# Performance work log

Measured on AMD Instinct MI355X. Metric: run time of the kernel, lower is better.

## Reference

```python
import jax, jax.numpy as jnp
import numpy as np

N_NODES = 50000


def _degree_norm(src, dst, n):
    # symmetric GCN normalization with self-loops already appended
    deg = jax.ops.segment_sum(jnp.ones(src.shape[0], jnp.float32), dst, num_segments=n)
    dinv = jnp.where(deg > 0, jax.lax.rsqrt(deg), 0.0)
    return dinv[src] * dinv[dst]  # [E_full]


def _gcn_layer(x, W, b, src, dst, norm, n):
    h = x @ W                                  # [N, out]
    msgs = h[src] * norm[:, None]              # gather + scale, [E_full, out]
    out = jax.ops.segment_sum(msgs, dst, num_segments=n)
    return out + b


def setup_inputs() -> dict:
    key = jax.random.key(0)
    k1, k2, k3, k4 = jax.random.split(key, 4)
    n, e, d_in, d_out = N_NODES, 800000, 256, 128
    x = jax.random.normal(k1, (n, d_in), jnp.float32)
    edge_index = jax.random.randint(k2, (2, e), 0, n, dtype=jnp.int64)
    W1 = jax.random.normal(k3, (d_in, 2 * d_out), jnp.float32) / np.sqrt(d_in)
    b1 = jnp.zeros((2 * d_out,), jnp.float32)
    W2 = jax.random.normal(k4, (2 * d_out, d_out), jnp.float32) / np.sqrt(2 * d_out)
    b2 = jnp.zeros((d_out,), jnp.float32)
    return {"x": x, "edge_index": edge_index, "W1": W1, "b1": b1, "W2": W2, "b2": b2}


def reference(x, edge_index, W1, b1, W2, b2):
    n = x.shape[0]
    loops = jnp.arange(n, dtype=edge_index.dtype)
    src = jnp.concatenate([edge_index[0], loops])
    dst = jnp.concatenate([edge_index[1], loops])
    norm = _degree_norm(src, dst, n)
    h = jax.nn.relu(_gcn_layer(x, W1, b1, src, dst, norm, n))
    h = jax.nn.relu(_gcn_layer(h, W2, b2, src, dst, norm, n))
    return h
```

## Files before the change

### kernel.cpp

```cpp
#include <hip/hip_runtime.h>
#include <hip/hip_bf16.h>


typedef __attribute__((ext_vector_type(8))) short bf16x8;
typedef __attribute__((ext_vector_type(8))) unsigned short u16x8;
typedef __attribute__((ext_vector_type(4))) float f32x4;

__device__ inline float bf2f(unsigned short u) {
    return __uint_as_float(((unsigned)u) << 16);
}
__device__ inline unsigned short f2bf(float f) {
    unsigned x = __float_as_uint(f);
    unsigned r = (x + 0x7fffu + ((x >> 16) & 1u)) >> 16;
    return (unsigned short)r;
}

#define NBIN 512

__global__ void degree_kernel(const int* __restrict__ dst, unsigned* __restrict__ deg, int E) {
    int e = blockIdx.x * blockDim.x + threadIdx.x;
    if (e < E) atomicAdd(&deg[dst[e]], 1u);
}

__global__ __launch_bounds__(256) void dinv_hist_kernel(const unsigned* __restrict__ deg,
                                                        float* __restrict__ dinv,
                                                        int* __restrict__ hist, int N) {
    __shared__ int lh[NBIN];
    const int t = threadIdx.x;
#pragma unroll
    for (int i = 0; i < NBIN / 256; i++) lh[t + i * 256] = 0;
    __syncthreads();
    int idx = blockIdx.x * 256 + t;
    if (idx < N) {
        unsigned d = deg[idx];
        dinv[idx] = rsqrtf((float)(d + 1u));
        int b = (int)d; if (b > NBIN - 1) b = NBIN - 1;
        atomicAdd(&lh[NBIN - 1 - b], 1);
    }
    __syncthreads();
#pragma unroll
    for (int i = 0; i < NBIN / 256; i++) {
        int v = lh[t + i * 256];
        if (v) atomicAdd(&hist[t + i * 256], v);
    }
}

__global__ void scan_bins_kernel(const int* __restrict__ hist,
                                 int* __restrict__ binstart,
                                 int* __restrict__ bincur,
                                 int* __restrict__ edgebase,
                                 int* __restrict__ rowptr, int N) {
    const int t = threadIdx.x;
    int cn = 0, ce = 0;
    for (int b = 0; b < NBIN; b += 64) {
        int i = b + t;
        int cnt = hist[i];
        int d = NBIN - 1 - i;
        int d8 = (d + 7) & ~7;
        int en = cnt * d8;
        int xn = cnt, xe = en;
#pragma unroll
        for (int off = 1; off < 64; off <<= 1) {
            int yn = __shfl_up(xn, off, 64);
            int ye = __shfl_up(xe, off, 64);
            if (t >= off) { xn += yn; xe += ye; }
        }
        binstart[i] = cn + xn - cnt;
        bincur[i]   = cn + xn - cnt;
        edgebase[i] = ce + xe - en;
        cn += __shfl(xn, 63, 64);
        ce += __shfl(xe, 63, 64);
    }
    if (t == 0) rowptr[N] = ce;
}

__global__ __launch_bounds__(256) void place_fused_kernel(
    const unsigned* __restrict__ deg,
    int* __restrict__ bincur,
    const int* __restrict__ binstart,
    const int* __restrict__ edgebase,
    int* __restrict__ perm,
    int* __restrict__ rowptr, int* __restrict__ cursor,
    unsigned short* __restrict__ col, int N) {
    __shared__ int lh[NBIN];
    __shared__ int base[NBIN];
    const int t = threadIdx.x;
#pragma unroll
    for (int i = 0; i < NBIN / 256; i++) lh[t + i * 256] = 0;
    __syncthreads();
    int idx = blockIdx.x * 256 + t;
    int bin = 0, lrank = 0;
    if (idx < N) {
        int b = (int)deg[idx]; if (b > NBIN - 1) b = NBIN - 1;
        bin = NBIN - 1 - b;
        lrank = atomicAdd(&lh[bin], 1);
    }
    __syncthreads();
#pragma unroll
    for (int i = 0; i < NBIN / 256; i++) {
        int v = lh[t + i * 256];
        if (v) base[t + i * 256] = atomicAdd(&bincur[t + i * 256], v);
    }
    __syncthreads();
    if (idx < N) {
        int pos = base[bin] + lrank;
        int d = NBIN - 1 - bin;
        int d8 = (d + 7) & ~7;
        int rp = edgebase[bin] + (pos - binstart[bin]) * d8;
        perm[pos] = idx;
        rowptr[pos] = rp;
        cursor[idx] = rp;
        for (int k = d; k < d8; k++) col[rp + k] = (unsigned short)N;
    }
}

__global__ __launch_bounds__(256) void fill_kernel(const int* __restrict__ src,
                                                   const int* __restrict__ dst,
                                                   int* __restrict__ cursor,
                                                   unsigned short* __restrict__ col, int E) {
    int e = blockIdx.x * blockDim.x + threadIdx.x;
    if (e < E) {
        int d = dst[e];
        int pos = atomicAdd(&cursor[d], 1);
        col[pos] = (unsigned short)src[e];
    }
}

__global__ __launch_bounds__(256) void convwt_pad_kernel(
    const float* __restrict__ W1, const float* __restrict__ W2,
    unsigned short* __restrict__ w1t, unsigned short* __restrict__ w2t,
    unsigned short* __restrict__ h1b, unsigned short* __restrict__ h2b,
    int DIN, int H, int DOUT, int Np1) {
    int id = blockIdx.x * 256 + threadIdx.x;
    int n1 = DIN * H;
    int n2 = H * DOUT;
    if (id < n1) {
        int k = id / H, n = id % H;
        w1t[(long)n * DIN + k] = f2bf(W1[id]);
    } else if (id < n1 + n2) {
        int q = id - n1;
        int k = q / DOUT, n = q % DOUT;
        w2t[(long)n * H + k] = f2bf(W2[q]);
    } else if (id < n1 + n2 + 384) {
        int q = id - n1 - n2;
        if (q < 256) {
            int c = q >> 5, f = q & 31;
            h1b[((size_t)c * Np1 + (Np1 - 1)) * 32 + f] = 0;
        } else {
            int q2 = q - 256;
            int c = q2 >> 5, f = q2 & 31;
            h2b[((size_t)c * Np1 + (Np1 - 1)) * 32 + f] = 0;
        }
    }
}

#define GBM 128
#define GBN 128
#define GBK 64
__global__ __launch_bounds__(256) void gemm_x_bf16(const float* __restrict__ X,
                                                   const float* __restrict__ dinv,
                                                   const unsigned short* __restrict__ BT,
                                                   unsigned short* __restrict__ C,
                                                   int M, int Nc, int K, int ldm) {
    __shared__ __align__(16) unsigned short As[GBM * GBK];
    __shared__ __align__(16) unsigned short Bs[GBN * GBK];
    const int t = threadIdx.x;
    const int lane = t & 63;
    const int w = t >> 6;
    const int row0 = blockIdx.x * GBM;
    const int col0 = blockIdx.y * GBN;
    const int rb = (w >> 1) * 64;
    const int cb = (w & 1) * 64;

    f32x4 acc[4][4] = {};

    for (int kb = 0; kb < K; kb += GBK) {
#pragma unroll
        for (int i = 0; i < 4; i++) {
            int p = i * 256 + t;
            int row = p >> 3;
            int slot = p & 7;
            int chunk = slot ^ (row & 7);
            int grow = row0 + row;
            if (grow >= M) grow = M - 1;
            const float* sp = X + (size_t)grow * K + kb + chunk * 8;
            f32x4 v0 = *(const f32x4*)sp;
            f32x4 v1 = *(const f32x4*)(sp + 4);
            float ds = dinv[grow];
            u16x8 o;
#pragma unroll
            for (int j = 0; j < 4; j++) { o[j] = f2bf(v0[j] * ds); o[j + 4] = f2bf(v1[j] * ds); }
            *(u16x8*)&As[p * 8] = o;
        }
#pragma unroll
        for (int i = 0; i < 4; i++) {
            int p = i * 256 + t;
            int row = p >> 3;
            int slot = p & 7;
            int chunk = slot ^ (row & 7);
            const unsigned short* src = BT + (size_t)(col0 + row) * K + kb + chunk * 8;
            __builtin_amdgcn_global_load_lds(
                (const __attribute__((address_space(1))) void*)src,
                (__attribute__((address_space(3))) void*)&Bs[p * 8], 16, 0, 0);
        }
        asm volatile("s_waitcnt vmcnt(0)" ::: "memory");
        __syncthreads();

#pragma unroll
        for (int ks = 0; ks < 2; ks++) {
            int kq = ks * 4 + (lane >> 4);
            int rsel = lane & 15;
            bf16x8 af[4], bfr[4];
#pragma unroll
            for (int mt = 0; mt < 4; mt++) {
                int m = rb + mt * 16 + rsel;
                int slot = kq ^ (m & 7);
                af[mt] = *(const bf16x8*)&As[m * GBK + slot * 8];
            }
#pragma unroll
            for (int nt = 0; nt < 4; nt++) {
                int n = cb + nt * 16 + rsel;
                int slot = kq ^ (n & 7);
                bfr[nt] = *(const bf16x8*)&Bs[n * GBK + slot * 8];
            }
#pragma unroll
            for (int mt = 0; mt < 4; mt++)
#pragma unroll
                for (int nt = 0; nt < 4; nt++)
                    acc[mt][nt] = __builtin_amdgcn_mfma_f32_16x16x32_bf16(
                        af[mt], bfr[nt], acc[mt][nt], 0, 0, 0);
        }
        __syncthreads();
    }

#pragma unroll
    for (int mt = 0; mt < 4; mt++) {
#pragma unroll
        for (int nt = 0; nt < 4; nt++) {
            int gcol = col0 + cb + nt * 16 + (lane & 15);
            int c = gcol >> 5;
            int fo = gcol & 31;
            int grow0 = row0 + rb + mt * 16 + 4 * (lane >> 4);
#pragma unroll
            for (int r = 0; r < 4; r++) {
                int g = grow0 + r;
                if (g < M)
                    C[((size_t)c * ldm + g) * 32 + fo] = f2bf(acc[mt][nt][r]);
            }
        }
    }
}

template <int CH>
__global__ __launch_bounds__(256) void gemm_bf16(const unsigned short* __restrict__ A,
                                                 const unsigned short* __restrict__ BT,
                                                 unsigned short* __restrict__ C,
                                                 int M, int Nc, int K, int ldm) {
    __shared__ __align__(16) unsigned short As[GBM * GBK];
    __shared__ __align__(16) unsigned short Bs[GBN * GBK];
    const int t = threadIdx.x;
    const int lane = t & 63;
    const int w = t >> 6;
    const int row0 = blockIdx.x * GBM;
    const int col0 = blockIdx.y * GBN;
    const int rb = (w >> 1) * 64;
    const int cb = (w & 1) * 64;

    f32x4 acc[4][4] = {};

    for (int kb = 0; kb < K; kb += GBK) {
#pragma unroll
        for (int i = 0; i < 4; i++) {
            int p = i * 256 + t;
            int row = p >> 3;
            int slot = p & 7;
            int chunk = slot ^ (row & 7);
            int grow = row0 + row;
            if (grow >= M) grow = M - 1;
            const unsigned short* src = A + (size_t)grow * K + kb + chunk * 8;
            __builtin_amdgcn_global_load_lds(
                (const __attribute__((address_space(1))) void*)src,
                (__attribute__((address_space(3))) void*)&As[p * 8], 16, 0, 0);
        }
#pragma unroll
        for (int i = 0; i < 4; i++) {
            int p = i * 256 + t;
            int row = p >> 3;
            int slot = p & 7;
            int chunk = slot ^ (row & 7);
            const unsigned short* src = BT + (size_t)(col0 + row) * K + kb + chunk * 8;
            __builtin_amdgcn_global_load_lds(
                (const __attribute__((address_space(1))) void*)src,
                (__attribute__((address_space(3))) void*)&Bs[p * 8], 16, 0, 0);
        }
        asm volatile("s_waitcnt vmcnt(0)" ::: "memory");
        __syncthreads();

#pragma unroll
        for (int ks = 0; ks < 2; ks++) {
            int kq = ks * 4 + (lane >> 4);
            int rsel = lane & 15;
            bf16x8 af[4], bfr[4];
#pragma unroll
            for (int mt = 0; mt < 4; mt++) {
                int m = rb + mt * 16 + rsel;
                int slot = kq ^ (m & 7);
                af[mt] = *(const bf16x8*)&As[m * GBK + slot * 8];
            }
#pragma unroll
            for (int nt = 0; nt < 4; nt++) {
                int n = cb + nt * 16 + rsel;
                int slot = kq ^ (n & 7);
                bfr[nt] = *(const bf16x8*)&Bs[n * GBK + slot * 8];
            }
#pragma unroll
            for (int mt = 0; mt < 4; mt++)
#pragma unroll
                for (int nt = 0; nt < 4; nt++)
                    acc[mt][nt] = __builtin_amdgcn_mfma_f32_16x16x32_bf16(
                        af[mt], bfr[nt], acc[mt][nt], 0, 0, 0);
        }
        __syncthreads();
    }

#pragma unroll
    for (int mt = 0; mt < 4; mt++) {
#pragma unroll
        for (int nt = 0; nt < 4; nt++) {
            int gcol = col0 + cb + nt * 16 + (lane & 15);
            int c = gcol / CH;
            int fo = gcol % CH;
            int grow0 = row0 + rb + mt * 16 + 4 * (lane >> 4);
#pragma unroll
            for (int r = 0; r < 4; r++) {
                int g = grow0 + r;
                if (g < M)
                    C[((size_t)c * ldm + g) * CH + fo] = f2bf(acc[mt][nt][r]);
            }
        }
    }
}

template <int CH, int NCH, bool OUT_BF16>
__global__ __launch_bounds__(512) void gather_cm_kernel(
    const unsigned short* __restrict__ h_cm,
    const int* __restrict__ rowptr,
    const unsigned short* __restrict__ col,
    const int* __restrict__ perm,
    const float* __restrict__ dinv,
    const float* __restrict__ bias,
    void* __restrict__ out,
    int Nn, int F) {
    constexpr int LF = CH / 8;
    constexpr int NS = 64 / LF;
    constexpr int NPB = NS * 8;
    const int chunk = blockIdx.x % NCH;
    const int g = blockIdx.x / NCH;
    const int w = threadIdx.x >> 6;
    const int lane = threadIdx.x & 63;
    const int fl = lane & (LF - 1);
    const int ns = lane / LF;
    const int idx = g * NPB + w * NS + ns;
    const bool valid = idx < Nn;
    const int cidx = valid ? idx : Nn - 1;
    const int node = perm[cidx];

    const unsigned short* hc = h_cm + (size_t)chunk * (Nn + 1) * CH;
    const int beg = rowptr[cidx];
    const int nit = (rowptr[cidx + 1] - beg) >> 3;
    const float ddst = dinv[node];
    const int fo = fl * 8;

    float a0[8] = {}, a1[8] = {};
    const unsigned short* cp = col + beg;
    u16x8 cv = *(const u16x8*)cp;
    for (int it = 0; it < nit; ++it) {
        int s0 = cv[0], s1 = cv[1], s2 = cv[2], s3 = cv[3];
        int s4 = cv[4], s5 = cv[5], s6 = cv[6], s7 = cv[7];
        u16x8 u0 = *(const u16x8*)(hc + s0 * CH + fo);
        u16x8 u1 = *(const u16x8*)(hc + s1 * CH + fo);
        u16x8 u2 = *(const u16x8*)(hc + s2 * CH + fo);
        u16x8 u3 = *(const u16x8*)(hc + s3 * CH + fo);
        u16x8 u4 = *(const u16x8*)(hc + s4 * CH + fo);
        u16x8 u5 = *(const u16x8*)(hc + s5 * CH + fo);
        u16x8 u6 = *(const u16x8*)(hc + s6 * CH + fo);
        u16x8 u7 = *(const u16x8*)(hc + s7 * CH + fo);
        cp += 8;
        cv = *(const u16x8*)cp;
#pragma unroll
        for (int j = 0; j < 8; j++) {
            a0[j] += (bf2f(u0[j]) + bf2f(u1[j])) + (bf2f(u2[j]) + bf2f(u3[j]));
            a1[j] += (bf2f(u4[j]) + bf2f(u5[j])) + (bf2f(u6[j]) + bf2f(u7[j]));
        }
    }

    if (valid) {
        u16x8 us = *(const u16x8*)(hc + node * CH + fo);
        const int f0g = chunk * CH + fo;
        f32x4 bv0 = *(const f32x4*)(bias + f0g);
        f32x4 bv1 = *(const f32x4*)(bias + f0g + 4);
        float v[8];
#pragma unroll
        for (int j = 0; j < 8; j++) {
            float b = (j < 4) ? bv0[j] : bv1[j - 4];
            float s = (a0[j] + a1[j]) + bf2f(us[j]);
            v[j] = fmaxf(fmaf(s, ddst, b), 0.f);
        }
        if (OUT_BF16) {
            u16x8 o;
#pragma unroll
            for (int j = 0; j < 8; j++) o[j] = f2bf(v[j] * ddst);
            *(u16x8*)((unsigned short*)out + (size_t)node * F + f0g) = o;
        } else {
            f32x4 o0, o1;
#pragma unroll
            for (int j = 0; j < 4; j++) { o0[j] = v[j]; o1[j] = v[j + 4]; }
            float* op = (float*)out + (size_t)node * F + f0g;
            *(f32x4*)op = o0;
            *(f32x4*)(op + 4) = o1;
        }
    }
}

extern "C" void kernel_launch(void* const* d_in, const int* in_sizes, int n_in,
                              void* d_out, int out_size, void* d_ws, size_t ws_size,
                              hipStream_t stream) {
    const float* x  = (const float*)d_in[0];
    const int* ei   = (const int*)d_in[1];
    const float* W1 = (const float*)d_in[2];
    const float* b1 = (const float*)d_in[3];
    const float* W2 = (const float*)d_in[4];
    const float* b2 = (const float*)d_in[5];

    const int DIN = 256;
    const int N = in_sizes[0] / DIN;
    const int E = in_sizes[1] / 2;
    const int H = in_sizes[3];
    const int DOUT = in_sizes[5];

    const int* src = ei;
    const int* dst = ei + E;

    char* ws = (char*)d_ws;
    unsigned* deg = (unsigned*)ws;                   ws += (size_t)N * 4;
    int* hist     = (int*)ws;                        ws += NBIN * 4;
    float* dinv   = (float*)ws;                      ws += (size_t)N * 4;
    int* rowptr   = (int*)ws;                        ws += (size_t)(N + 4) * 4;
    int* binstart = (int*)ws;                        ws += NBIN * 4;
    int* bincur   = (int*)ws;                        ws += NBIN * 4;
    int* edgebase = (int*)ws;                        ws += NBIN * 4;
    int* perm     = (int*)ws;                        ws += (size_t)N * 4;
    int* cursor   = (int*)ws;                        ws += (size_t)N * 4;
    unsigned short* col = (unsigned short*)ws;       ws += (size_t)(E + 8 * N + 64) * 2;
    unsigned short* w1t = (unsigned short*)ws;       ws += (size_t)DIN * H * 2;
    unsigned short* w2t = (unsigned short*)ws;       ws += (size_t)H * DOUT * 2;
    unsigned short* h1b = (unsigned short*)ws;       ws += (size_t)(N + 1) * H * 2 + 1024;
    unsigned short* y1b = (unsigned short*)ws;       ws += (size_t)N * H * 2;
    unsigned short* h2b = (unsigned short*)ws;       ws += (size_t)(N + 1) * DOUT * 2 + 1024;
    float* outp = (float*)d_out;

    hipMemsetAsync(deg, 0, (size_t)N * 4 + NBIN * 4, stream);
    degree_kernel<<<(E + 255) / 256, 256, 0, stream>>>(dst, deg, E);
    dinv_hist_kernel<<<(N + 255) / 256, 256, 0, stream>>>(deg, dinv, hist, N);
    scan_bins_kernel<<<1, 64, 0, stream>>>(hist, binstart, bincur, edgebase, rowptr, N);
    place_fused_kernel<<<(N + 255) / 256, 256, 0, stream>>>(
        deg, bincur, binstart, edgebase, perm, rowptr, cursor, col, N);
    fill_kernel<<<(E + 255) / 256, 256, 0, stream>>>(src, dst, cursor, col, E);

    {
        int tot = DIN * H + H * DOUT + 384;
        convwt_pad_kernel<<<(tot + 255) / 256, 256, 0, stream>>>(
            W1, W2, w1t, w2t, h1b, h2b, DIN, H, DOUT, N + 1);
    }

    {
        dim3 grid((N + GBM - 1) / GBM, H / GBN);
        gemm_x_bf16<<<grid, 256, 0, stream>>>(x, dinv, w1t, h1b, N, H, DIN, N + 1);
    }
    {
        constexpr int NPB1 = (64 / (32 / 8)) * 8;
        gather_cm_kernel<32, 8, true><<<8 * ((N + NPB1 - 1) / NPB1), 512, 0, stream>>>(
            h1b, rowptr, col, perm, dinv, b1, y1b, N, H);
    }

    {
        dim3 grid((N + GBM - 1) / GBM, DOUT / GBN);
        gemm_bf16<32><<<grid, 256, 0, stream>>>(y1b, w2t, h2b, N, DOUT, H, N + 1);
    }
    {
        constexpr int NPB2 = (64 / (32 / 8)) * 8;
        gather_cm_kernel<32, 4, false><<<4 * ((N + NPB2 - 1) / NPB2), 512, 0, stream>>>(
            h2b, rowptr, col, perm, dinv, b2, outp, N, DOUT);
    }
}
```

Measured before the change: 313.5 us.

## Fold bin scan into placement kernel and compute full layer-1 width per GEMM block

The single-wave scan_bins kernel is removed. Each place_fused block now recomputes the prefix scan of the degree histogram into shared memory and reserves slots through a zeroed binres counter, which saves one launch and its serial dependency. The first-layer GEMM now has each block compute both 128-column tiles of the 256-wide output, so the fp32 X tile is loaded and converted to bf16 once instead of twice. The cost is double the accumulator registers and B shared memory, which may lower occupancy, plus a redundant scan in every placement block.

```diff
diff --git a/kernel.cpp b/kernel.cpp
--- a/kernel.cpp
+++ b/kernel.cpp
@@ -45,49 +45,42 @@
     }
 }
 
-__global__ void scan_bins_kernel(const int* __restrict__ hist,
-                                 int* __restrict__ binstart,
-                                 int* __restrict__ bincur,
-                                 int* __restrict__ edgebase,
-                                 int* __restrict__ rowptr, int N) {
-    const int t = threadIdx.x;
-    int cn = 0, ce = 0;
-    for (int b = 0; b < NBIN; b += 64) {
-        int i = b + t;
-        int cnt = hist[i];
-        int d = NBIN - 1 - i;
-        int d8 = (d + 7) & ~7;
-        int en = cnt * d8;
-        int xn = cnt, xe = en;
-#pragma unroll
-        for (int off = 1; off < 64; off <<= 1) {
-            int yn = __shfl_up(xn, off, 64);
-            int ye = __shfl_up(xe, off, 64);
-            if (t >= off) { xn += yn; xe += ye; }
-        }
-        binstart[i] = cn + xn - cnt;
-        bincur[i]   = cn + xn - cnt;
-        edgebase[i] = ce + xe - en;
-        cn += __shfl(xn, 63, 64);
-        ce += __shfl(xe, 63, 64);
-    }
-    if (t == 0) rowptr[N] = ce;
-}
-
 __global__ __launch_bounds__(256) void place_fused_kernel(
     const unsigned* __restrict__ deg,
-    int* __restrict__ bincur,
-    const int* __restrict__ binstart,
-    const int* __restrict__ edgebase,
+    const int* __restrict__ hist,
+    int* __restrict__ binres,
     int* __restrict__ perm,
     int* __restrict__ rowptr, int* __restrict__ cursor,
     unsigned short* __restrict__ col, int N) {
     __shared__ int lh[NBIN];
     __shared__ int base[NBIN];
+    __shared__ int binstartL[NBIN];
+    __shared__ int edgebaseL[NBIN];
     const int t = threadIdx.x;
 #pragma unroll
     for (int i = 0; i < NBIN / 256; i++) lh[t + i * 256] = 0;
     __syncthreads();
+    if (t < 64) {
+        int cn = 0, ce = 0;
+        for (int b = 0; b < NBIN; b += 64) {
+            int i = b + t;
+            int cnt = hist[i];
+            int d = NBIN - 1 - i;
+            int d8 = (d + 7) & ~7;
+            int en = cnt * d8;
+            int xn = cnt, xe = en;
+#pragma unroll
+            for (int off = 1; off < 64; off <<= 1) {
+                int yn = __shfl_up(xn, off, 64);
+                int ye = __shfl_up(xe, off, 64);
+                if (t >= off) { xn += yn; xe += ye; }
+            }
+            binstartL[i] = cn + xn - cnt;
+            edgebaseL[i] = ce + xe - en;
+            cn += __shfl(xn, 63, 64);
+            ce += __shfl(xe, 63, 64);
+        }
+    }
     int idx = blockIdx.x * 256 + t;
     int bin = 0, lrank = 0;
     if (idx < N) {
@@ -96,17 +89,19 @@
         lrank = atomicAdd(&lh[bin], 1);
     }
     __syncthreads();
+    if (blockIdx.x == 0 && t == 0) rowptr[N] = edgebaseL[NBIN - 1];
 #pragma unroll
     for (int i = 0; i < NBIN / 256; i++) {
         int v = lh[t + i * 256];
-        if (v) base[t + i * 256] = atomicAdd(&bincur[t + i * 256], v);
+        if (v) base[t + i * 256] = binstartL[t + i * 256] +
+                                   atomicAdd(&binres[t + i * 256], v);
     }
     __syncthreads();
     if (idx < N) {
         int pos = base[bin] + lrank;
         int d = NBIN - 1 - bin;
         int d8 = (d + 7) & ~7;
-        int rp = edgebase[bin] + (pos - binstart[bin]) * d8;
+        int rp = edgebaseL[bin] + (pos - binstartL[bin]) * d8;
         perm[pos] = idx;
         rowptr[pos] = rp;
         cursor[idx] = rp;
@@ -161,18 +156,17 @@
                                                    const float* __restrict__ dinv,
                                                    const unsigned short* __restrict__ BT,
                                                    unsigned short* __restrict__ C,
-                                                   int M, int Nc, int K, int ldm) {
+                                                   int M, int K, int ldm) {
     __shared__ __align__(16) unsigned short As[GBM * GBK];
-    __shared__ __align__(16) unsigned short Bs[GBN * GBK];
+    __shared__ __align__(16) unsigned short Bs[2][GBN * GBK];
     const int t = threadIdx.x;
     const int lane = t & 63;
     const int w = t >> 6;
     const int row0 = blockIdx.x * GBM;
-    const int col0 = blockIdx.y * GBN;
     const int rb = (w >> 1) * 64;
     const int cb = (w & 1) * 64;
 
-    f32x4 acc[4][4] = {};
+    f32x4 acc[2][4][4] = {};
 
     for (int kb = 0; kb < K; kb += GBK) {
 #pragma unroll
@@ -193,16 +187,18 @@
             *(u16x8*)&As[p * 8] = o;
         }
 #pragma unroll
-        for (int i = 0; i < 4; i++) {
-            int p = i * 256 + t;
-            int row = p >> 3;
-            int slot = p & 7;
-            int chunk = slot ^ (row & 7);
-            const unsigned short* src = BT + (size_t)(col0 + row) * K + kb + chunk * 8;
-            __builtin_amdgcn_global_load_lds(
-                (const __attribute__((address_space(1))) void*)src,
-                (__attribute__((address_space(3))) void*)&Bs[p * 8], 16, 0, 0);
-        }
+        for (int ct = 0; ct < 2; ct++)
+#pragma unroll
+            for (int i = 0; i < 4; i++) {
+                int p = i * 256 + t;
+                int row = p >> 3;
+                int slot = p & 7;
+                int chunk = slot ^ (row & 7);
+                const unsigned short* src = BT + (size_t)(ct * GBN + row) * K + kb + chunk * 8;
+                __builtin_amdgcn_global_load_lds(
+                    (const __attribute__((address_space(1))) void*)src,
+                    (__attribute__((address_space(3))) void*)&Bs[ct][p * 8], 16, 0, 0);
+            }
         asm volatile("s_waitcnt vmcnt(0)" ::: "memory");
         __syncthreads();
 
@@ -210,7 +206,7 @@
         for (int ks = 0; ks < 2; ks++) {
             int kq = ks * 4 + (lane >> 4);
             int rsel = lane & 15;
-            bf16x8 af[4], bfr[4];
+            bf16x8 af[4];
 #pragma unroll
             for (int mt = 0; mt < 4; mt++) {
                 int m = rb + mt * 16 + rsel;
@@ -218,37 +214,42 @@
                 af[mt] = *(const bf16x8*)&As[m * GBK + slot * 8];
             }
 #pragma unroll
+            for (int ct = 0; ct < 2; ct++) {
+                bf16x8 bfr[4];
+#pragma unroll
+                for (int nt = 0; nt < 4; nt++) {
+                    int n = cb + nt * 16 + rsel;
+                    int slot = kq ^ (n & 7);
+                    bfr[nt] = *(const bf16x8*)&Bs[ct][n * GBK + slot * 8];
+                }
+#pragma unroll
+                for (int mt = 0; mt < 4; mt++)
+#pragma unroll
+                    for (int nt = 0; nt < 4; nt++)
+                        acc[ct][mt][nt] = __builtin_amdgcn_mfma_f32_16x16x32_bf16(
+                            af[mt], bfr[nt], acc[ct][mt][nt], 0, 0, 0);
+            }
+        }
+        __syncthreads();
+    }
+
+#pragma unroll
+    for (int ct = 0; ct < 2; ct++)
+#pragma unroll
+        for (int mt = 0; mt < 4; mt++)
+#pragma unroll
             for (int nt = 0; nt < 4; nt++) {
-                int n = cb + nt * 16 + rsel;
-                int slot = kq ^ (n & 7);
-                bfr[nt] = *(const bf16x8*)&Bs[n * GBK + slot * 8];
-            }
-#pragma unroll
-            for (int mt = 0; mt < 4; mt++)
-#pragma unroll
-                for (int nt = 0; nt < 4; nt++)
-                    acc[mt][nt] = __builtin_amdgcn_mfma_f32_16x16x32_bf16(
-                        af[mt], bfr[nt], acc[mt][nt], 0, 0, 0);
-        }
-        __syncthreads();
-    }
-
-#pragma unroll
-    for (int mt = 0; mt < 4; mt++) {
-#pragma unroll
-        for (int nt = 0; nt < 4; nt++) {
-            int gcol = col0 + cb + nt * 16 + (lane & 15);
-            int c = gcol >> 5;
-            int fo = gcol & 31;
-            int grow0 = row0 + rb + mt * 16 + 4 * (lane >> 4);
-#pragma unroll
-            for (int r = 0; r < 4; r++) {
-                int g = grow0 + r;
-                if (g < M)
-                    C[((size_t)c * ldm + g) * 32 + fo] = f2bf(acc[mt][nt][r]);
-            }
-        }
-    }
+                int gcol = ct * GBN + cb + nt * 16 + (lane & 15);
+                int c = gcol >> 5;
+                int fo = gcol & 31;
+                int grow0 = row0 + rb + mt * 16 + 4 * (lane >> 4);
+#pragma unroll
+                for (int r = 0; r < 4; r++) {
+                    int g = grow0 + r;
+                    if (g < M)
+                        C[((size_t)c * ldm + g) * 32 + fo] = f2bf(acc[ct][mt][nt][r]);
+                }
+            }
 }
 
 template <int CH>
@@ -444,11 +445,9 @@
     char* ws = (char*)d_ws;
     unsigned* deg = (unsigned*)ws;                   ws += (size_t)N * 4;
     int* hist     = (int*)ws;                        ws += NBIN * 4;
+    int* binres   = (int*)ws;                        ws += NBIN * 4;
     float* dinv   = (float*)ws;                      ws += (size_t)N * 4;
     int* rowptr   = (int*)ws;                        ws += (size_t)(N + 4) * 4;
-    int* binstart = (int*)ws;                        ws += NBIN * 4;
-    int* bincur   = (int*)ws;                        ws += NBIN * 4;
-    int* edgebase = (int*)ws;                        ws += NBIN * 4;
     int* perm     = (int*)ws;                        ws += (size_t)N * 4;
     int* cursor   = (int*)ws;                        ws += (size_t)N * 4;
     unsigned short* col = (unsigned short*)ws;       ws += (size_t)(E + 8 * N + 64) * 2;
@@ -459,12 +458,11 @@
     unsigned short* h2b = (unsigned short*)ws;       ws += (size_t)(N + 1) * DOUT * 2 + 1024;
     float* outp = (float*)d_out;
 
-    hipMemsetAsync(deg, 0, (size_t)N * 4 + NBIN * 4, stream);
+    hipMemsetAsync(deg, 0, (size_t)N * 4 + (size_t)2 * NBIN * 4, stream);
     degree_kernel<<<(E + 255) / 256, 256, 0, stream>>>(dst, deg, E);
     dinv_hist_kernel<<<(N + 255) / 256, 256, 0, stream>>>(deg, dinv, hist, N);
-    scan_bins_kernel<<<1, 64, 0, stream>>>(hist, binstart, bincur, edgebase, rowptr, N);
     place_fused_kernel<<<(N + 255) / 256, 256, 0, stream>>>(
-        deg, bincur, binstart, edgebase, perm, rowptr, cursor, col, N);
+        deg, hist, binres, perm, rowptr, cursor, col, N);
     fill_kernel<<<(E + 255) / 256, 256, 0, stream>>>(src, dst, cursor, col, E);
 
     {
@@ -474,8 +472,8 @@
     }
 
     {
-        dim3 grid((N + GBM - 1) / GBM, H / GBN);
-        gemm_x_bf16<<<grid, 256, 0, stream>>>(x, dinv, w1t, h1b, N, H, DIN, N + 1);
+        dim3 grid((N + GBM - 1) / GBM, 1);
+        gemm_x_bf16<<<grid, 256, 0, stream>>>(x, dinv, w1t, h1b, N, DIN, N + 1);
     }
     {
         constexpr int NPB1 = (64 / (32 / 8)) * 8;
```

Result: no change. 315.4 us, median of 2 (+0.6%).
